# Kernel optimization log

Measured on AMD Instinct MI355X. Metric: run time of the kernel, lower is better.

## Reference

```python
import jax, jax.numpy as jnp
import numpy as np

B, C, D_BB, D = 16384, 4, 2048, 512
MAX_NORM = 3.0
LN_EPS = 1e-5


def setup_inputs() -> dict:
    key = jax.random.key(0)
    ks = jax.random.split(key, 6)
    return {
        "thumbnails": jax.random.normal(ks[0], (B, C, D_BB), dtype=jnp.float32),
        # nn.Linear(backbone_dim, hidden_dim): weight [D, D_BB], bias [D]
        "proj_w": jax.random.normal(ks[1], (D, D_BB), dtype=jnp.float32) / np.float32(np.sqrt(D_BB)),
        "proj_b": jnp.zeros((D,), dtype=jnp.float32),
        # per-camera LayerNorm affine params [C, D]
        "gamma": jnp.ones((C, D), dtype=jnp.float32),
        "beta": jnp.zeros((C, D), dtype=jnp.float32),
        # per-camera SwiGLU weights (no bias), torch Linear convention [out, in]
        "w_gate": jax.random.normal(ks[2], (C, D, D), dtype=jnp.float32) / np.float32(np.sqrt(D)),
        "w_val": jax.random.normal(ks[3], (C, D, D), dtype=jnp.float32) / np.float32(np.sqrt(D)),
        # per-camera output proj D->36 (zero-init in module; small random for a useful baseline)
        "w_out": jax.random.normal(ks[4], (C, 36, D), dtype=jnp.float32) * np.float32(0.02),
    }


def _expm66(A):
    """Matrix exponential of [..., 6, 6] matrices with ||A||_F <= MAX_NORM.

    Scaling-and-squaring with a fixed order-12 Taylor series. After scaling by
    2^-4, ||A/16|| <= 0.1875, so the order-12 truncation error is << fp32 eps.
    Matches torch.linalg.matrix_exp to fp32 precision and is fully transposable.
    """
    s = 4  # number of squarings
    As = A * jnp.asarray(1.0 / (2 ** s), A.dtype)
    I = jnp.broadcast_to(jnp.eye(6, dtype=A.dtype), A.shape)
    E = I
    term = I
    for k in range(1, 13):
        term = jnp.matmul(term, As) * jnp.asarray(1.0 / k, A.dtype)
        E = E + term
    for _ in range(s):
        E = jnp.matmul(E, E)
    return E


def reference(thumbnails, proj_w, proj_b, gamma, beta, w_gate, w_val, w_out):
    # thumbnail projection: [B,C,D_BB] @ [D,D_BB]^T -> [B,C,D]
    reg = jnp.einsum('bce,de->bcd', thumbnails, proj_w) + proj_b
    # per-camera LayerNorm (biased variance, as in torch)
    mu = jnp.mean(reg, axis=-1, keepdims=True)
    var = jnp.var(reg, axis=-1, keepdims=True)
    xn = (reg - mu) * jax.lax.rsqrt(var + LN_EPS) * gamma + beta  # gamma/beta broadcast [C,D]
    # SwiGLU (per-camera weights)
    gate = jnp.einsum('bcd,cfd->bcf', xn, w_gate)
    val = jnp.einsum('bcd,cfd->bcf', xn, w_val)
    h = jax.nn.silu(gate) * val
    # project to Lie algebra, skew-symmetrize
    A = jnp.einsum('bcf,cof->bco', h, w_out).reshape(B, C, 6, 6)
    A = A - jnp.swapaxes(A, -1, -2)
    # Frobenius-norm clip to MAX_NORM
    frob = jnp.sqrt(jnp.sum(A * A, axis=(-2, -1), keepdims=True))
    A = A * (jnp.minimum(frob, MAX_NORM) / jnp.maximum(frob, 1e-8))
    # matrix exponential -> orthogonal deltaM, returned as [C, B, 6, 6]
    dM = _expm66(A)
    return jnp.swapaxes(dM, 0, 1)
```

## Files before the change

kernel.cpp:

```cpp
#include <hip/hip_runtime.h>
#include <cstdint>
#include <cstddef>


#define B_SZ   16384
#define C_CAM  4
#define DBB    2048
#define D_H    512

typedef __attribute__((ext_vector_type(8))) short  bf16x8;
typedef __attribute__((ext_vector_type(4))) float  f32x4;

__device__ __forceinline__ unsigned short f2b(float f) {
    union { float f; unsigned u; } v; v.f = f;
    unsigned r = (v.u + 0x7FFFu + ((v.u >> 16) & 1u)) >> 16;
    return (unsigned short)r;
}
__device__ __forceinline__ float b2f(unsigned short u) {
    union { unsigned u; float f; } v; v.u = ((unsigned)u) << 16;
    return v.f;
}

#define GLDS(g, l) __builtin_amdgcn_global_load_lds( \
    (const __attribute__((address_space(1))) unsigned int*)(g), \
    (__attribute__((address_space(3))) unsigned int*)(l), 16, 0, 0)

__global__ void k_cvt(const float* __restrict__ src, unsigned short* __restrict__ dst, int n) {
    int i = blockIdx.x * blockDim.x + threadIdx.x;
    int stride = gridDim.x * blockDim.x;
    for (; i < n; i += stride) dst[i] = f2b(src[i]);
}

__global__ __launch_bounds__(256)
void k_cvt8(const float* __restrict__ src, unsigned short* __restrict__ dst, long n8) {
    long i = (long)blockIdx.x * blockDim.x + threadIdx.x;
    if (i >= n8) return;
    const float4 a = ((const float4*)src)[i * 2];
    const float4 b = ((const float4*)src)[i * 2 + 1];
    unsigned short o[8] = {f2b(a.x), f2b(a.y), f2b(a.z), f2b(a.w),
                           f2b(b.x), f2b(b.y), f2b(b.z), f2b(b.w)};
    ((uint4*)dst)[i] = *(const uint4*)o;
}

__global__ void k_cvt_wout(const float* __restrict__ src, unsigned short* __restrict__ dst) {
    int i = blockIdx.x * blockDim.x + threadIdx.x;
    if (i >= C_CAM * 48 * D_H) return;
    int col = i & (D_H - 1);
    int row = (i >> 9) % 48;
    int c   = i / (48 * D_H);
    dst[i] = (row < 36) ? f2b(src[((size_t)c * 36 + row) * D_H + col]) : (unsigned short)0;
}

__global__ __launch_bounds__(256)
void k_projb(const unsigned short* __restrict__ A, const unsigned short* __restrict__ Bw,
             const float* __restrict__ bias, unsigned short* __restrict__ regb) {
    __shared__ unsigned short lsA[128 * 32];
    __shared__ unsigned short lsB[128 * 32];
    const int t = threadIdx.x;
    const int tile_n = blockIdx.x * 128;
    const int tile_m = blockIdx.y * 128;
    const int w = t >> 6, l = t & 63, lr = l & 15, quad = l >> 4;
    const int wm = (w >> 1) * 64, wn = (w & 1) * 64;

    f32x4 acc[4][4];
#pragma unroll
    for (int i = 0; i < 4; i++)
#pragma unroll
        for (int j = 0; j < 4; j++) acc[i][j] = (f32x4){0.f, 0.f, 0.f, 0.f};

    const int srow = l >> 2, scol = (l & 3) * 8;
    const unsigned short* baseA = A  + (size_t)(tile_m + w * 32 + srow) * DBB + scol;
    const unsigned short* baseB = Bw + (size_t)(tile_n + w * 32 + srow) * DBB + scol;
    unsigned short* ldsAw = &lsA[w * 32 * 32];
    unsigned short* ldsBw = &lsB[w * 32 * 32];

    for (int kt = 0; kt < DBB / 32; ++kt) {
        __syncthreads();
        GLDS(baseA + kt * 32,            ldsAw);
        GLDS(baseA + kt * 32 + 16 * DBB, ldsAw + 16 * 32);
        GLDS(baseB + kt * 32,            ldsBw);
        GLDS(baseB + kt * 32 + 16 * DBB, ldsBw + 16 * 32);
        __syncthreads();
        bf16x8 af[4], bfr[4];
#pragma unroll
        for (int i = 0; i < 4; i++)
            af[i] = *(const bf16x8*)(&lsA[(wm + i * 16 + lr) * 32 + quad * 8]);
#pragma unroll
        for (int j = 0; j < 4; j++)
            bfr[j] = *(const bf16x8*)(&lsB[(wn + j * 16 + lr) * 32 + quad * 8]);
#pragma unroll
        for (int i = 0; i < 4; i++)
#pragma unroll
            for (int j = 0; j < 4; j++)
                acc[i][j] = __builtin_amdgcn_mfma_f32_16x16x32_bf16(af[i], bfr[j], acc[i][j], 0, 0, 0);
    }
#pragma unroll
    for (int j = 0; j < 4; j++) {
        const int col = tile_n + wn + j * 16 + lr;
        const float bv = bias[col];
#pragma unroll
        for (int i = 0; i < 4; i++)
#pragma unroll
            for (int r = 0; r < 4; r++) {
                const int row = tile_m + wm + i * 16 + quad * 4 + r;
                regb[(size_t)row * D_H + col] = f2b(acc[i][j][r] + bv);
            }
    }
}

__global__ __launch_bounds__(256)
void k_projf(const float* __restrict__ A, const unsigned short* __restrict__ Bw,
             const float* __restrict__ bias, unsigned short* __restrict__ regb) {
    __shared__ unsigned short lsA[128 * 72];
    __shared__ unsigned short lsB[128 * 72];
    const int t = threadIdx.x;
    const int tile_n = blockIdx.x * 128;
    const int tile_m = blockIdx.y * 128;
    const int w = t >> 6, l = t & 63, lr = l & 15, quad = l >> 4;
    const int wm = (w >> 1) * 64, wn = (w & 1) * 64;

    f32x4 acc[4][4];
#pragma unroll
    for (int i = 0; i < 4; i++)
#pragma unroll
        for (int j = 0; j < 4; j++) acc[i][j] = (f32x4){0.f, 0.f, 0.f, 0.f};

    const int ar = t >> 4, ac = (t & 15) * 4;
    const int br = t >> 3, bc = (t & 7) * 8;

    for (int kt = 0; kt < DBB / 64; ++kt) {
        __syncthreads();
#pragma unroll
        for (int p = 0; p < 8; p++) {
            const int row = p * 16 + ar;
            const float4 v = *(const float4*)(A + (size_t)(tile_m + row) * DBB + kt * 64 + ac);
            unsigned p0 = (unsigned)f2b(v.x) | ((unsigned)f2b(v.y) << 16);
            unsigned p1 = (unsigned)f2b(v.z) | ((unsigned)f2b(v.w) << 16);
            *(uint2*)(&lsA[row * 72 + ac]) = make_uint2(p0, p1);
        }
#pragma unroll
        for (int p = 0; p < 4; p++) {
            const int row = p * 32 + br;
            *(uint4*)(&lsB[row * 72 + bc]) =
                *(const uint4*)(Bw + (size_t)(tile_n + row) * DBB + kt * 64 + bc);
        }
        __syncthreads();
#pragma unroll
        for (int kk = 0; kk < 2; ++kk) {
            bf16x8 af[4], bfr[4];
#pragma unroll
            for (int i = 0; i < 4; i++)
                af[i] = *(const bf16x8*)(&lsA[(wm + i * 16 + lr) * 72 + kk * 32 + quad * 8]);
#pragma unroll
            for (int j = 0; j < 4; j++)
                bfr[j] = *(const bf16x8*)(&lsB[(wn + j * 16 + lr) * 72 + kk * 32 + quad * 8]);
#pragma unroll
            for (int i = 0; i < 4; i++)
#pragma unroll
                for (int j = 0; j < 4; j++)
                    acc[i][j] = __builtin_amdgcn_mfma_f32_16x16x32_bf16(af[i], bfr[j], acc[i][j], 0, 0, 0);
        }
    }
#pragma unroll
    for (int j = 0; j < 4; j++) {
        const int col = tile_n + wn + j * 16 + lr;
        const float bv = bias[col];
#pragma unroll
        for (int i = 0; i < 4; i++)
#pragma unroll
            for (int r = 0; r < 4; r++) {
                const int row = tile_m + wm + i * 16 + quad * 4 + r;
                regb[(size_t)row * D_H + col] = f2b(acc[i][j][r] + bv);
            }
    }
}

__global__ __launch_bounds__(256)
void k_ln(const unsigned short* __restrict__ regb, const float* __restrict__ gamma,
          const float* __restrict__ beta, unsigned short* __restrict__ xnb) {
    const int t = threadIdx.x;
    const int wave = t >> 6, l = t & 63;
    const int r = blockIdx.x * 4 + wave;
    const int c = r & 3, b = r >> 2;

    const uint4 pk = *(const uint4*)(regb + (size_t)r * D_H + l * 8);
    const unsigned short* ps = (const unsigned short*)&pk;
    float x[8];
#pragma unroll
    for (int j = 0; j < 8; j++) x[j] = b2f(ps[j]);

    float s = 0.f, ss = 0.f;
#pragma unroll
    for (int j = 0; j < 8; j++) { s += x[j]; ss += x[j] * x[j]; }
#pragma unroll
    for (int off = 32; off > 0; off >>= 1) {
        s  += __shfl_xor(s, off);
        ss += __shfl_xor(ss, off);
    }
    const float mu  = s * (1.0f / 512.0f);
    const float var = ss * (1.0f / 512.0f) - mu * mu;
    const float rs  = rsqrtf(var + 1e-5f);

    unsigned short o[8];
#pragma unroll
    for (int j = 0; j < 8; j++) {
        const int d = l * 8 + j;
        o[j] = f2b((x[j] - mu) * rs * gamma[c * D_H + d] + beta[c * D_H + d]);
    }
    *(uint4*)(xnb + ((size_t)c * B_SZ + b) * D_H + l * 8) = *(const uint4*)o;
}

__global__ __launch_bounds__(256)
void k_swiglu(const unsigned short* __restrict__ xnb, const unsigned short* __restrict__ wg,
              const unsigned short* __restrict__ wv, unsigned short* __restrict__ hb) {
    __shared__ unsigned short lsA[128 * 32];
    __shared__ unsigned short lsG[128 * 32];
    __shared__ unsigned short lsV[128 * 32];
    const int t = threadIdx.x;
    const int tile_n = blockIdx.x * 128;
    const int tile_m = blockIdx.y * 128;
    const int cam = blockIdx.z;
    const unsigned short* Ac = xnb + (size_t)cam * B_SZ * D_H;
    const unsigned short* Gc = wg + (size_t)cam * D_H * D_H;
    const unsigned short* Vc = wv + (size_t)cam * D_H * D_H;
    const int w = t >> 6, l = t & 63, lr = l & 15, quad = l >> 4;
    const int wm = (w >> 1) * 64, wn = (w & 1) * 64;

    f32x4 ag[4][4], av[4][4];
#pragma unroll
    for (int i = 0; i < 4; i++)
#pragma unroll
        for (int j = 0; j < 4; j++) { ag[i][j] = (f32x4){0.f,0.f,0.f,0.f}; av[i][j] = (f32x4){0.f,0.f,0.f,0.f}; }

    const int srow = l >> 2, scol = (l & 3) * 8;
    const unsigned short* baseA = Ac + (size_t)(tile_m + w * 32 + srow) * D_H + scol;
    const unsigned short* baseG = Gc + (size_t)(tile_n + w * 32 + srow) * D_H + scol;
    const unsigned short* baseV = Vc + (size_t)(tile_n + w * 32 + srow) * D_H + scol;
    unsigned short* ldsAw = &lsA[w * 32 * 32];
    unsigned short* ldsGw = &lsG[w * 32 * 32];
    unsigned short* ldsVw = &lsV[w * 32 * 32];

    for (int kt = 0; kt < D_H / 32; ++kt) {
        __syncthreads();
        GLDS(baseA + kt * 32,            ldsAw);
        GLDS(baseA + kt * 32 + 16 * D_H, ldsAw + 16 * 32);
        GLDS(baseG + kt * 32,            ldsGw);
        GLDS(baseG + kt * 32 + 16 * D_H, ldsGw + 16 * 32);
        GLDS(baseV + kt * 32,            ldsVw);
        GLDS(baseV + kt * 32 + 16 * D_H, ldsVw + 16 * 32);
        __syncthreads();
        bf16x8 af[4];
#pragma unroll
        for (int i = 0; i < 4; i++)
            af[i] = *(const bf16x8*)(&lsA[(wm + i * 16 + lr) * 32 + quad * 8]);
#pragma unroll
        for (int j = 0; j < 4; j++) {
            bf16x8 gf = *(const bf16x8*)(&lsG[(wn + j * 16 + lr) * 32 + quad * 8]);
            bf16x8 vf = *(const bf16x8*)(&lsV[(wn + j * 16 + lr) * 32 + quad * 8]);
#pragma unroll
            for (int i = 0; i < 4; i++) {
                ag[i][j] = __builtin_amdgcn_mfma_f32_16x16x32_bf16(af[i], gf, ag[i][j], 0, 0, 0);
                av[i][j] = __builtin_amdgcn_mfma_f32_16x16x32_bf16(af[i], vf, av[i][j], 0, 0, 0);
            }
        }
    }
#pragma unroll
    for (int i = 0; i < 4; i++)
#pragma unroll
        for (int j = 0; j < 4; j++)
#pragma unroll
            for (int r = 0; r < 4; r++) {
                const int row = tile_m + wm + i * 16 + quad * 4 + r;
                const int col = tile_n + wn + j * 16 + lr;
                const float g = ag[i][j][r], v = av[i][j][r];
                const float h = g * v / (1.0f + __expf(-g));
                hb[((size_t)cam * B_SZ + row) * D_H + col] = f2b(h);
            }
}

__global__ __launch_bounds__(256)
void k_outproj(const unsigned short* __restrict__ hb, const unsigned short* __restrict__ wo,
               float* __restrict__ Abuf) {
    __shared__ unsigned short lsA[128 * 32];
    __shared__ unsigned short lsB[48 * 32];
    const int t = threadIdx.x;
    const int tile_m = blockIdx.y * 128;
    const int cam = blockIdx.z;
    const unsigned short* Ac = hb + (size_t)cam * B_SZ * D_H;
    const unsigned short* Bc = wo + (size_t)cam * 48 * D_H;
    const int w = t >> 6, l = t & 63, lr = l & 15, quad = l >> 4;
    const int srow = l >> 2, scol = (l & 3) * 8;

    f32x4 acc[2][3];
#pragma unroll
    for (int i = 0; i < 2; i++)
#pragma unroll
        for (int j = 0; j < 3; j++) acc[i][j] = (f32x4){0.f,0.f,0.f,0.f};

    const unsigned short* baseA = Ac + (size_t)(tile_m + w * 32 + srow) * D_H + scol;
    const unsigned short* baseB = Bc + (size_t)(w * 16 + srow) * D_H + scol;
    unsigned short* ldsAw = &lsA[w * 32 * 32];
    unsigned short* ldsBw = &lsB[w * 16 * 32];

    for (int kt = 0; kt < D_H / 32; ++kt) {
        __syncthreads();
        GLDS(baseA + kt * 32,            ldsAw);
        GLDS(baseA + kt * 32 + 16 * D_H, ldsAw + 16 * 32);
        if (w < 3) GLDS(baseB + kt * 32, ldsBw);
        __syncthreads();
        bf16x8 af[2], bfr[3];
#pragma unroll
        for (int i = 0; i < 2; i++)
            af[i] = *(const bf16x8*)(&lsA[(w * 32 + i * 16 + lr) * 32 + quad * 8]);
#pragma unroll
        for (int j = 0; j < 3; j++)
            bfr[j] = *(const bf16x8*)(&lsB[(j * 16 + lr) * 32 + quad * 8]);
#pragma unroll
        for (int i = 0; i < 2; i++)
#pragma unroll
            for (int j = 0; j < 3; j++)
                acc[i][j] = __builtin_amdgcn_mfma_f32_16x16x32_bf16(af[i], bfr[j], acc[i][j], 0, 0, 0);
    }
#pragma unroll
    for (int i = 0; i < 2; i++)
#pragma unroll
        for (int j = 0; j < 3; j++)
#pragma unroll
            for (int r = 0; r < 4; r++) {
                const int col = j * 16 + lr;
                if (col < 36) {
                    const int row = tile_m + w * 32 + i * 16 + quad * 4 + r;
                    Abuf[((size_t)cam * B_SZ + row) * 36 + col] = acc[i][j][r];
                }
            }
}

__global__ __launch_bounds__(128)
void k_expm(const float* __restrict__ Abuf, float* __restrict__ out) {
    const int gid = blockIdx.x * blockDim.x + threadIdx.x;
    if (gid >= B_SZ * C_CAM) return;
    const float* Ap = Abuf + (size_t)gid * 36;

    float a[36];
#pragma unroll
    for (int i = 0; i < 36; i++) a[i] = Ap[i];

    float S[36];
#pragma unroll
    for (int i = 0; i < 6; i++)
#pragma unroll
        for (int j = 0; j < 6; j++) S[i * 6 + j] = a[i * 6 + j] - a[j * 6 + i];

    float fr2 = 0.f;
#pragma unroll
    for (int i = 0; i < 36; i++) fr2 += S[i] * S[i];
    const float fr = sqrtf(fr2);
    const float sc = fminf(fr, 3.0f) / fmaxf(fr, 1e-8f) * 0.0625f;

    float As[36];
#pragma unroll
    for (int i = 0; i < 36; i++) As[i] = S[i] * sc;

    float E[36], T[36], tmp[36];
#pragma unroll
    for (int i = 0; i < 36; i++) { E[i] = (i % 7 == 0) ? 1.f : 0.f; T[i] = E[i]; }

#pragma unroll
    for (int k = 1; k <= 12; k++) {
        const float invk = 1.0f / (float)k;
#pragma unroll
        for (int i = 0; i < 6; i++)
#pragma unroll
            for (int j = 0; j < 6; j++) {
                float sum = 0.f;
#pragma unroll
                for (int q = 0; q < 6; q++) sum += T[i * 6 + q] * As[q * 6 + j];
                tmp[i * 6 + j] = sum * invk;
            }
#pragma unroll
        for (int i = 0; i < 36; i++) { T[i] = tmp[i]; E[i] += tmp[i]; }
    }
#pragma unroll
    for (int sq = 0; sq < 4; sq++) {
#pragma unroll
        for (int i = 0; i < 6; i++)
#pragma unroll
            for (int j = 0; j < 6; j++) {
                float sum = 0.f;
#pragma unroll
                for (int q = 0; q < 6; q++) sum += E[i * 6 + q] * E[q * 6 + j];
                tmp[i * 6 + j] = sum;
            }
#pragma unroll
        for (int i = 0; i < 36; i++) E[i] = tmp[i];
    }

    float* op = out + (size_t)gid * 36;
#pragma unroll
    for (int i = 0; i < 36; i++) op[i] = E[i];
}

extern "C" void kernel_launch(void* const* d_in, const int* in_sizes, int n_in,
                              void* d_out, int out_size, void* d_ws, size_t ws_size,
                              hipStream_t stream) {
    const float* thumb  = (const float*)d_in[0];
    const float* proj_w = (const float*)d_in[1];
    const float* proj_b = (const float*)d_in[2];
    const float* gamma  = (const float*)d_in[3];
    const float* beta   = (const float*)d_in[4];
    const float* w_gate = (const float*)d_in[5];
    const float* w_val  = (const float*)d_in[6];
    const float* w_out  = (const float*)d_in[7];

    char* ws = (char*)d_ws;
    const size_t FAST_WS = 409141248ULL;

    if (ws_size >= FAST_WS) {
        unsigned short* Abf  = (unsigned short*)(ws);
        unsigned short* regb = (unsigned short*)(ws + 268435456);
        unsigned short* xnb  = (unsigned short*)(ws + 335544320);
        unsigned short* hb   = (unsigned short*)(ws);
        float*          Abuf = (float*)(ws + 268435456);
        unsigned short* pwb  = (unsigned short*)(ws + 402653184);
        unsigned short* wgb  = (unsigned short*)(ws + 404750336);
        unsigned short* wvb  = (unsigned short*)(ws + 406847488);
        unsigned short* wob  = (unsigned short*)(ws + 408944640);

        hipLaunchKernelGGL(k_cvt8, dim3(65536), dim3(256), 0, stream,
                           thumb, Abf, (long)B_SZ * C_CAM * DBB / 8);
        hipLaunchKernelGGL(k_cvt, dim3(1024), dim3(256), 0, stream, proj_w, pwb, D_H * DBB);
        hipLaunchKernelGGL(k_cvt, dim3(1024), dim3(256), 0, stream, w_gate, wgb, C_CAM * D_H * D_H);
        hipLaunchKernelGGL(k_cvt, dim3(1024), dim3(256), 0, stream, w_val, wvb, C_CAM * D_H * D_H);
        hipLaunchKernelGGL(k_cvt_wout, dim3((C_CAM * 48 * D_H + 255) / 256), dim3(256), 0, stream, w_out, wob);

        hipLaunchKernelGGL(k_projb, dim3(4, 512), dim3(256), 0, stream, Abf, pwb, proj_b, regb);
        hipLaunchKernelGGL(k_ln, dim3(B_SZ * C_CAM / 4), dim3(256), 0, stream, regb, gamma, beta, xnb);
        hipLaunchKernelGGL(k_swiglu, dim3(4, 128, 4), dim3(256), 0, stream, xnb, wgb, wvb, hb);
        hipLaunchKernelGGL(k_outproj, dim3(1, 128, 4), dim3(256), 0, stream, hb, wob, Abuf);
        hipLaunchKernelGGL(k_expm, dim3(B_SZ * C_CAM / 128), dim3(128), 0, stream, Abuf, (float*)d_out);
    } else {
        unsigned short* regb = (unsigned short*)(ws + 0);
        unsigned short* xnb  = (unsigned short*)(ws + 67108864);
        unsigned short* hb   = (unsigned short*)(ws + 0);
        float*          Abuf = (float*)(ws + 67108864);
        unsigned short* pwb  = (unsigned short*)(ws + 134217728);
        unsigned short* wgb  = (unsigned short*)(ws + 136314880);
        unsigned short* wvb  = (unsigned short*)(ws + 138412032);
        unsigned short* wob  = (unsigned short*)(ws + 140509184);

        hipLaunchKernelGGL(k_cvt, dim3(1024), dim3(256), 0, stream, proj_w, pwb, D_H * DBB);
        hipLaunchKernelGGL(k_cvt, dim3(1024), dim3(256), 0, stream, w_gate, wgb, C_CAM * D_H * D_H);
        hipLaunchKernelGGL(k_cvt, dim3(1024), dim3(256), 0, stream, w_val, wvb, C_CAM * D_H * D_H);
        hipLaunchKernelGGL(k_cvt_wout, dim3((C_CAM * 48 * D_H + 255) / 256), dim3(256), 0, stream, w_out, wob);

        hipLaunchKernelGGL(k_projf, dim3(4, 512), dim3(256), 0, stream, thumb, pwb, proj_b, regb);
        hipLaunchKernelGGL(k_ln, dim3(B_SZ * C_CAM / 4), dim3(256), 0, stream, regb, gamma, beta, xnb);
        hipLaunchKernelGGL(k_swiglu, dim3(4, 128, 4), dim3(256), 0, stream, xnb, wgb, wvb, hb);
        hipLaunchKernelGGL(k_outproj, dim3(1, 128, 4), dim3(256), 0, stream, hb, wob, Abuf);
        hipLaunchKernelGGL(k_expm, dim3(B_SZ * C_CAM / 128), dim3(128), 0, stream, Abuf, (float*)d_out);
    }
}
```

Before: 1.183 ms.

## Fuse fp32-to-bf16 thumbnail conversion into projection GEMM via direct LDS loads

Removes the separate pass that converted the full thumbnail tensor to bf16 in workspace. The projection GEMM now streams fp32 thumbnails into LDS with global_load_lds and converts to bf16 in registers while building MFMA fragments. This avoids writing and re-reading a large intermediate buffer. It also merges the three weight-conversion launches into one vectorized kernel with a cheaper packed-bf16 conversion that rounds ties away from zero instead of to even. The cost is double the fp32 LDS traffic per K-tile, extra conversion ALU work inside the GEMM loop, and a small change in rounding.

```diff
diff --git a/kernel.cpp b/kernel.cpp
--- a/kernel.cpp
+++ b/kernel.cpp
@@ -20,26 +20,29 @@
     union { unsigned u; float f; } v; v.u = ((unsigned)u) << 16;
     return v.f;
 }
+__device__ __forceinline__ unsigned pkbf(float a, float b) {
+    union { float f; unsigned u; } x, y; x.f = a; y.f = b;
+    return __builtin_amdgcn_perm(y.u + 0x8000u, x.u + 0x8000u, 0x07060302u);
+}
 
 #define GLDS(g, l) __builtin_amdgcn_global_load_lds( \
     (const __attribute__((address_space(1))) unsigned int*)(g), \
     (__attribute__((address_space(3))) unsigned int*)(l), 16, 0, 0)
 
-__global__ void k_cvt(const float* __restrict__ src, unsigned short* __restrict__ dst, int n) {
+__global__ __launch_bounds__(256)
+void k_cvtw(const float* __restrict__ pw, const float* __restrict__ wg,
+            const float* __restrict__ wv, unsigned short* __restrict__ opw,
+            unsigned short* __restrict__ owg, unsigned short* __restrict__ owv) {
+    const int N8 = (D_H * DBB) / 8;
     int i = blockIdx.x * blockDim.x + threadIdx.x;
-    int stride = gridDim.x * blockDim.x;
-    for (; i < n; i += stride) dst[i] = f2b(src[i]);
-}
-
-__global__ __launch_bounds__(256)
-void k_cvt8(const float* __restrict__ src, unsigned short* __restrict__ dst, long n8) {
-    long i = (long)blockIdx.x * blockDim.x + threadIdx.x;
-    if (i >= n8) return;
-    const float4 a = ((const float4*)src)[i * 2];
-    const float4 b = ((const float4*)src)[i * 2 + 1];
-    unsigned short o[8] = {f2b(a.x), f2b(a.y), f2b(a.z), f2b(a.w),
-                           f2b(b.x), f2b(b.y), f2b(b.z), f2b(b.w)};
-    ((uint4*)dst)[i] = *(const uint4*)o;
+    const float* s; unsigned short* d; int j;
+    if (i < N8)          { s = pw; d = opw; j = i; }
+    else if (i < 2 * N8) { s = wg; d = owg; j = i - N8; }
+    else                 { s = wv; d = owv; j = i - 2 * N8; }
+    const float4 a = ((const float4*)s)[j * 2];
+    const float4 b = ((const float4*)s)[j * 2 + 1];
+    unsigned o[4] = {pkbf(a.x, a.y), pkbf(a.z, a.w), pkbf(b.x, b.y), pkbf(b.z, b.w)};
+    ((uint4*)d)[j] = *(const uint4*)o;
 }
 
 __global__ void k_cvt_wout(const float* __restrict__ src, unsigned short* __restrict__ dst) {
@@ -52,9 +55,9 @@
 }
 
 __global__ __launch_bounds__(256)
-void k_projb(const unsigned short* __restrict__ A, const unsigned short* __restrict__ Bw,
+void k_proj2(const float* __restrict__ A, const unsigned short* __restrict__ Bw,
              const float* __restrict__ bias, unsigned short* __restrict__ regb) {
-    __shared__ unsigned short lsA[128 * 32];
+    __shared__ float lsAf[2 * 128 * 16];
     __shared__ unsigned short lsB[128 * 32];
     const int t = threadIdx.x;
     const int tile_n = blockIdx.x * 128;
@@ -68,23 +71,37 @@
 #pragma unroll
         for (int j = 0; j < 4; j++) acc[i][j] = (f32x4){0.f, 0.f, 0.f, 0.f};
 
-    const int srow = l >> 2, scol = (l & 3) * 8;
-    const unsigned short* baseA = A  + (size_t)(tile_m + w * 32 + srow) * DBB + scol;
-    const unsigned short* baseB = Bw + (size_t)(tile_n + w * 32 + srow) * DBB + scol;
-    unsigned short* ldsAw = &lsA[w * 32 * 32];
+    const int arow = l >> 2, akc = l & 3;
+    const float* baseA = A + (size_t)(tile_m + w * 32 + arow) * DBB + akc * 4;
+    float* ldsA_w = lsAf + (w * 32) * 16;
+
+    const unsigned short* baseB = Bw + (size_t)(tile_n + w * 32 + arow) * DBB + akc * 8;
     unsigned short* ldsBw = &lsB[w * 32 * 32];
 
+    const int h = quad >> 1, q1 = quad & 1;
+
     for (int kt = 0; kt < DBB / 32; ++kt) {
         __syncthreads();
-        GLDS(baseA + kt * 32,            ldsAw);
-        GLDS(baseA + kt * 32 + 16 * DBB, ldsAw + 16 * 32);
+        const float* ga = baseA + kt * 32;
+        GLDS(ga,                  ldsA_w);
+        GLDS(ga + 16,             ldsA_w + 2048);
+        GLDS(ga + 16 * DBB,       ldsA_w + 256);
+        GLDS(ga + 16 * DBB + 16,  ldsA_w + 2048 + 256);
         GLDS(baseB + kt * 32,            ldsBw);
         GLDS(baseB + kt * 32 + 16 * DBB, ldsBw + 16 * 32);
         __syncthreads();
+
         bf16x8 af[4], bfr[4];
 #pragma unroll
-        for (int i = 0; i < 4; i++)
-            af[i] = *(const bf16x8*)(&lsA[(wm + i * 16 + lr) * 32 + quad * 8]);
+        for (int i = 0; i < 4; i++) {
+            const float* ap = lsAf + h * 2048 + (wm + i * 16 + lr) * 16 + q1 * 8;
+            const f32x4 lo = *(const f32x4*)ap;
+            const f32x4 hi = *(const f32x4*)(ap + 4);
+            union { unsigned u[4]; bf16x8 v; } cv;
+            cv.u[0] = pkbf(lo[0], lo[1]); cv.u[1] = pkbf(lo[2], lo[3]);
+            cv.u[2] = pkbf(hi[0], hi[1]); cv.u[3] = pkbf(hi[2], hi[3]);
+            af[i] = cv.v;
+        }
 #pragma unroll
         for (int j = 0; j < 4; j++)
             bfr[j] = *(const bf16x8*)(&lsB[(wn + j * 16 + lr) * 32 + quad * 8]);
@@ -93,73 +110,6 @@
 #pragma unroll
             for (int j = 0; j < 4; j++)
                 acc[i][j] = __builtin_amdgcn_mfma_f32_16x16x32_bf16(af[i], bfr[j], acc[i][j], 0, 0, 0);
-    }
-#pragma unroll
-    for (int j = 0; j < 4; j++) {
-        const int col = tile_n + wn + j * 16 + lr;
-        const float bv = bias[col];
-#pragma unroll
-        for (int i = 0; i < 4; i++)
-#pragma unroll
-            for (int r = 0; r < 4; r++) {
-                const int row = tile_m + wm + i * 16 + quad * 4 + r;
-                regb[(size_t)row * D_H + col] = f2b(acc[i][j][r] + bv);
-            }
-    }
-}
-
-__global__ __launch_bounds__(256)
-void k_projf(const float* __restrict__ A, const unsigned short* __restrict__ Bw,
-             const float* __restrict__ bias, unsigned short* __restrict__ regb) {
-    __shared__ unsigned short lsA[128 * 72];
-    __shared__ unsigned short lsB[128 * 72];
-    const int t = threadIdx.x;
-    const int tile_n = blockIdx.x * 128;
-    const int tile_m = blockIdx.y * 128;
-    const int w = t >> 6, l = t & 63, lr = l & 15, quad = l >> 4;
-    const int wm = (w >> 1) * 64, wn = (w & 1) * 64;
-
-    f32x4 acc[4][4];
-#pragma unroll
-    for (int i = 0; i < 4; i++)
-#pragma unroll
-        for (int j = 0; j < 4; j++) acc[i][j] = (f32x4){0.f, 0.f, 0.f, 0.f};
-
-    const int ar = t >> 4, ac = (t & 15) * 4;
-    const int br = t >> 3, bc = (t & 7) * 8;
-
-    for (int kt = 0; kt < DBB / 64; ++kt) {
-        __syncthreads();
-#pragma unroll
-        for (int p = 0; p < 8; p++) {
-            const int row = p * 16 + ar;
-            const float4 v = *(const float4*)(A + (size_t)(tile_m + row) * DBB + kt * 64 + ac);
-            unsigned p0 = (unsigned)f2b(v.x) | ((unsigned)f2b(v.y) << 16);
-            unsigned p1 = (unsigned)f2b(v.z) | ((unsigned)f2b(v.w) << 16);
-            *(uint2*)(&lsA[row * 72 + ac]) = make_uint2(p0, p1);
-        }
-#pragma unroll
-        for (int p = 0; p < 4; p++) {
-            const int row = p * 32 + br;
-            *(uint4*)(&lsB[row * 72 + bc]) =
-                *(const uint4*)(Bw + (size_t)(tile_n + row) * DBB + kt * 64 + bc);
-        }
-        __syncthreads();
-#pragma unroll
-        for (int kk = 0; kk < 2; ++kk) {
-            bf16x8 af[4], bfr[4];
-#pragma unroll
-            for (int i = 0; i < 4; i++)
-                af[i] = *(const bf16x8*)(&lsA[(wm + i * 16 + lr) * 72 + kk * 32 + quad * 8]);
-#pragma unroll
-            for (int j = 0; j < 4; j++)
-                bfr[j] = *(const bf16x8*)(&lsB[(wn + j * 16 + lr) * 72 + kk * 32 + quad * 8]);
-#pragma unroll
-            for (int i = 0; i < 4; i++)
-#pragma unroll
-                for (int j = 0; j < 4; j++)
-                    acc[i][j] = __builtin_amdgcn_mfma_f32_16x16x32_bf16(af[i], bfr[j], acc[i][j], 0, 0, 0);
-        }
     }
 #pragma unroll
     for (int j = 0; j < 4; j++) {
@@ -413,50 +363,22 @@
     const float* w_out  = (const float*)d_in[7];
 
     char* ws = (char*)d_ws;
-    const size_t FAST_WS = 409141248ULL;
-
-    if (ws_size >= FAST_WS) {
-        unsigned short* Abf  = (unsigned short*)(ws);
-        unsigned short* regb = (unsigned short*)(ws + 268435456);
-        unsigned short* xnb  = (unsigned short*)(ws + 335544320);
-        unsigned short* hb   = (unsigned short*)(ws);
-        float*          Abuf = (float*)(ws + 268435456);
-        unsigned short* pwb  = (unsigned short*)(ws + 402653184);
-        unsigned short* wgb  = (unsigned short*)(ws + 404750336);
-        unsigned short* wvb  = (unsigned short*)(ws + 406847488);
-        unsigned short* wob  = (unsigned short*)(ws + 408944640);
-
-        hipLaunchKernelGGL(k_cvt8, dim3(65536), dim3(256), 0, stream,
-                           thumb, Abf, (long)B_SZ * C_CAM * DBB / 8);
-        hipLaunchKernelGGL(k_cvt, dim3(1024), dim3(256), 0, stream, proj_w, pwb, D_H * DBB);
-        hipLaunchKernelGGL(k_cvt, dim3(1024), dim3(256), 0, stream, w_gate, wgb, C_CAM * D_H * D_H);
-        hipLaunchKernelGGL(k_cvt, dim3(1024), dim3(256), 0, stream, w_val, wvb, C_CAM * D_H * D_H);
-        hipLaunchKernelGGL(k_cvt_wout, dim3((C_CAM * 48 * D_H + 255) / 256), dim3(256), 0, stream, w_out, wob);
-
-        hipLaunchKernelGGL(k_projb, dim3(4, 512), dim3(256), 0, stream, Abf, pwb, proj_b, regb);
-        hipLaunchKernelGGL(k_ln, dim3(B_SZ * C_CAM / 4), dim3(256), 0, stream, regb, gamma, beta, xnb);
-        hipLaunchKernelGGL(k_swiglu, dim3(4, 128, 4), dim3(256), 0, stream, xnb, wgb, wvb, hb);
-        hipLaunchKernelGGL(k_outproj, dim3(1, 128, 4), dim3(256), 0, stream, hb, wob, Abuf);
-        hipLaunchKernelGGL(k_expm, dim3(B_SZ * C_CAM / 128), dim3(128), 0, stream, Abuf, (float*)d_out);
-    } else {
-        unsigned short* regb = (unsigned short*)(ws + 0);
-        unsigned short* xnb  = (unsigned short*)(ws + 67108864);
-        unsigned short* hb   = (unsigned short*)(ws + 0);
-        float*          Abuf = (float*)(ws + 67108864);
-        unsigned short* pwb  = (unsigned short*)(ws + 134217728);
-        unsigned short* wgb  = (unsigned short*)(ws + 136314880);
-        unsigned short* wvb  = (unsigned short*)(ws + 138412032);
-        unsigned short* wob  = (unsigned short*)(ws + 140509184);
-
-        hipLaunchKernelGGL(k_cvt, dim3(1024), dim3(256), 0, stream, proj_w, pwb, D_H * DBB);
-        hipLaunchKernelGGL(k_cvt, dim3(1024), dim3(256), 0, stream, w_gate, wgb, C_CAM * D_H * D_H);
-        hipLaunchKernelGGL(k_cvt, dim3(1024), dim3(256), 0, stream, w_val, wvb, C_CAM * D_H * D_H);
-        hipLaunchKernelGGL(k_cvt_wout, dim3((C_CAM * 48 * D_H + 255) / 256), dim3(256), 0, stream, w_out, wob);
-
-        hipLaunchKernelGGL(k_projf, dim3(4, 512), dim3(256), 0, stream, thumb, pwb, proj_b, regb);
-        hipLaunchKernelGGL(k_ln, dim3(B_SZ * C_CAM / 4), dim3(256), 0, stream, regb, gamma, beta, xnb);
-        hipLaunchKernelGGL(k_swiglu, dim3(4, 128, 4), dim3(256), 0, stream, xnb, wgb, wvb, hb);
-        hipLaunchKernelGGL(k_outproj, dim3(1, 128, 4), dim3(256), 0, stream, hb, wob, Abuf);
-        hipLaunchKernelGGL(k_expm, dim3(B_SZ * C_CAM / 128), dim3(128), 0, stream, Abuf, (float*)d_out);
-    }
-}
+    unsigned short* regb = (unsigned short*)(ws + 0);
+    unsigned short* xnb  = (unsigned short*)(ws + 67108864);
+    unsigned short* hb   = (unsigned short*)(ws + 0);
+    float*          Abuf = (float*)(ws + 67108864);
+    unsigned short* pwb  = (unsigned short*)(ws + 134217728);
+    unsigned short* wgb  = (unsigned short*)(ws + 136314880);
+    unsigned short* wvb  = (unsigned short*)(ws + 138412032);
+    unsigned short* wob  = (unsigned short*)(ws + 140509184);
+
+    hipLaunchKernelGGL(k_cvtw, dim3(3 * (D_H * DBB / 8) / 256), dim3(256), 0, stream,
+                       proj_w, w_gate, w_val, pwb, wgb, wvb);
+    hipLaunchKernelGGL(k_cvt_wout, dim3((C_CAM * 48 * D_H + 255) / 256), dim3(256), 0, stream, w_out, wob);
+
+    hipLaunchKernelGGL(k_proj2, dim3(4, 512), dim3(256), 0, stream, thumb, pwb, proj_b, regb);
+    hipLaunchKernelGGL(k_ln, dim3(B_SZ * C_CAM / 4), dim3(256), 0, stream, regb, gamma, beta, xnb);
+    hipLaunchKernelGGL(k_swiglu, dim3(4, 128, 4), dim3(256), 0, stream, xnb, wgb, wvb, hb);
+    hipLaunchKernelGGL(k_outproj, dim3(1, 128, 4), dim3(256), 0, stream, hb, wob, Abuf);
+    hipLaunchKernelGGL(k_expm, dim3(B_SZ * C_CAM / 128), dim3(128), 0, stream, Abuf, (float*)d_out);
+}
```

Result: slower. 1.247 ms (+5.4%).
